# Kernel tuning notes

Hardware: AMD Instinct MI355X
Metric: run time of the kernel (lower is better)

The kernel has to match this reference:

```python
import jax, jax.numpy as jnp
import numpy as np

HEAD_NUM = 16


def setup_inputs() -> dict:
    key = jax.random.key(0)
    k1, k2, k3, k4 = jax.random.split(key, 4)
    B, S, E = 8, 1024, 1024
    inputs = jax.random.normal(k1, (B, S, E), dtype=jnp.float32)
    W_Query = jax.random.normal(k2, (E, E), dtype=jnp.float32) * 0.05
    W_Key = jax.random.normal(k3, (E, E), dtype=jnp.float32) * 0.05
    W_Value = jax.random.normal(k4, (E, E), dtype=jnp.float32) * 0.05
    return {"inputs": inputs, "W_Query": W_Query, "W_Key": W_Key, "W_Value": W_Value}


def reference(inputs, W_Query, W_Key, W_Value):
    B, S, E = inputs.shape
    H = HEAD_NUM
    D = E // H
    # QKV projections: [B,S,E] @ [E,E] -> [B,S,E]
    q = jnp.einsum('bse,ef->bsf', inputs, W_Query).reshape(B, S, H, D)
    k = jnp.einsum('bse,ef->bsf', inputs, W_Key).reshape(B, S, H, D)
    v = jnp.einsum('bse,ef->bsf', inputs, W_Value).reshape(B, S, H, D)
    # NOTE: original has NO 1/sqrt(D) scaling.
    scores = jnp.einsum('bihd,bjhd->bhij', q, k)  # [B,H,S,S]
    att = jax.nn.softmax(scores, axis=-1)
    out = jnp.einsum('bhij,bjhd->bihd', att, v).reshape(B, S, E)
    return jax.nn.relu(out)
```

## Files before the change

### kernel.cpp

```cpp
#include <hip/hip_runtime.h>
#include <cstdint>
#include <cstddef>

#define B_ 8
#define S_ 1024
#define E_ 1024
#define H_ 16
#define D_ 64
#define M_ (B_*S_)

typedef _Float16 f16;
typedef __attribute__((ext_vector_type(8))) _Float16 f16x8;
typedef __attribute__((ext_vector_type(4))) _Float16 f16x4;
typedef __attribute__((ext_vector_type(4))) float  f32x4;
typedef __attribute__((ext_vector_type(16))) float f32x16;
typedef __attribute__((ext_vector_type(4))) int    int4v;
typedef __attribute__((ext_vector_type(2))) int    int2v;

__device__ __forceinline__ f32x4 mfma16(f16x8 a, f16x8 b, f32x4 c) {
  return __builtin_amdgcn_mfma_f32_16x16x32_f16(a, b, c, 0, 0, 0);
}
__device__ __forceinline__ f32x16 mfma32(f16x8 a, f16x8 b, f32x16 c) {
  return __builtin_amdgcn_mfma_f32_32x32x16_f16(a, b, c, 0, 0, 0);
}
__device__ __forceinline__ void gll16(const f16* g, f16* l) {
  __builtin_amdgcn_global_load_lds(
      (const __attribute__((address_space(1))) void*)g,
      (__attribute__((address_space(3))) void*)l, 16, 0, 0);
}
__device__ __forceinline__ int pkrtz(float lo, float hi) {
  return __builtin_bit_cast(int, __builtin_amdgcn_cvt_pkrtz(lo, hi));
}

__global__ __launch_bounds__(256) void presplit_kernel(
    const float* __restrict__ X, f16* __restrict__ Xf) {
  size_t i = ((size_t)blockIdx.x * 256 + threadIdx.x) * 8;
  f32x4 v0 = *(const f32x4*)&X[i];
  f32x4 v1 = *(const f32x4*)&X[i + 4];
  f16x8 hv;
#pragma unroll
  for (int j = 0; j < 4; ++j) {
    hv[j] = (f16)v0[j];
    hv[j + 4] = (f16)v1[j];
  }
  *(f16x8*)&Xf[i] = hv;
}

__global__ __launch_bounds__(512) void wt_conv3_kernel(
    const float* __restrict__ Wq, const float* __restrict__ Wk,
    const float* __restrict__ Wv, f16* __restrict__ oq, f16* __restrict__ ok,
    f16* __restrict__ ov) {
  const float* W = blockIdx.z == 0 ? Wq : (blockIdx.z == 1 ? Wk : Wv);
  f16* o = blockIdx.z == 0 ? oq : (blockIdx.z == 1 ? ok : ov);
  const float scl = blockIdx.z == 0 ? 1.4426950408889634f : 1.0f;
  __shared__ float t[64][65];
  const int f0 = blockIdx.x * 64, e0 = blockIdx.y * 64;
  const int tx = threadIdx.x, ty = threadIdx.y;
#pragma unroll
  for (int j = 0; j < 8; ++j)
    t[ty + 8 * j][tx] = W[(size_t)(e0 + ty + 8 * j) * E_ + f0 + tx];
  __syncthreads();
#pragma unroll
  for (int j = 0; j < 8; ++j)
    o[(size_t)(f0 + ty + 8 * j) * E_ + e0 + tx] =
        (f16)(t[tx][ty + 8 * j] * scl);
}

__global__ __launch_bounds__(256) void gemm_qkv_kernel(
    const f16* __restrict__ Xf,
    const f16* __restrict__ Wq, const f16* __restrict__ Wk,
    const f16* __restrict__ Wv,
    f16* __restrict__ Qf, f16* __restrict__ Kf, f16* __restrict__ Vt) {
  __shared__ f16 sA[128][64], sB[128][64];
  const int bid = blockIdx.x;
  const int xcd = bid & 7, idx = bid >> 3;
  const int mb = xcd * 8 + idx / 24;
  const int nb = idx % 24;
  const int z = nb >> 3;
  const int n0 = (nb & 7) * 128, m0 = mb * 128;
  const f16* __restrict__ Bt = z == 0 ? Wq : (z == 1 ? Wk : Wv);
  const int tid = threadIdx.x;
  const int lane = tid & 63, w = tid >> 6;
  const int wm = (w >> 1) * 64, wn = (w & 1) * 64;
  const int fr = lane & 15, fg = lane >> 4;
  f32x4 acc[4][4] = {};
  for (int k0 = 0; k0 < E_; k0 += 64) {
#pragma unroll
    for (int i = 0; i < 4; ++i) {
      int ci = tid + i * 256;
      int r = ci >> 3, cl = ci & 7;
      int cs = (cl ^ (r & 7)) * 8;
      gll16(Xf + (size_t)(m0 + r) * E_ + k0 + cs, &sA[0][0] + ci * 8);
      gll16(Bt + (size_t)(n0 + r) * E_ + k0 + cs, &sB[0][0] + ci * 8);
    }
    __syncthreads();
#pragma unroll
    for (int kh2 = 0; kh2 < 2; ++kh2) {
      f16x8 ah[4];
#pragma unroll
      for (int mi = 0; mi < 4; ++mi) {
        int rA = wm + mi * 16 + fr;
        ah[mi] = *(const f16x8*)&sA[rA][(((kh2 * 4 + fg) ^ (rA & 7))) * 8];
      }
#pragma unroll
      for (int ni = 0; ni < 4; ++ni) {
        int rB = wn + ni * 16 + fr;
        f16x8 bh = *(const f16x8*)&sB[rB][(((kh2 * 4 + fg) ^ (rB & 7))) * 8];
#pragma unroll
        for (int mi = 0; mi < 4; ++mi)
          acc[mi][ni] = mfma16(ah[mi], bh, acc[mi][ni]);
      }
    }
    __syncthreads();
  }
  if (z < 2) {
    f16* Of = z == 0 ? Qf : Kf;
#pragma unroll
    for (int mi = 0; mi < 4; ++mi)
#pragma unroll
      for (int ni = 0; ni < 4; ++ni)
#pragma unroll
        for (int r = 0; r < 4; ++r) {
          int row = m0 + wm + mi * 16 + (lane >> 4) * 4 + r;
          int col = n0 + wn + ni * 16 + fr;
          int bb = row >> 10, s = row & 1023;
          int hd = col >> 6, d = col & 63;
          Of[((size_t)(bb * H_ + hd) * S_ + s) * D_ + d] = (f16)acc[mi][ni][r];
        }
  } else {
#pragma unroll
    for (int mi = 0; mi < 4; ++mi)
#pragma unroll
      for (int ni = 0; ni < 4; ++ni) {
        int row = m0 + wm + mi * 16 + (lane >> 4) * 4;
        int col = n0 + wn + ni * 16 + fr;
        int bb = row >> 10, s = row & 1023;
        int hd = col >> 6, d = col & 63;
        f16x4 p;
#pragma unroll
        for (int r = 0; r < 4; ++r) p[r] = (f16)acc[mi][ni][r];
        *(f16x4*)&Vt[((size_t)(bb * H_ + hd) * D_ + d) * S_ + s] = p;
      }
  }
}

__global__ __launch_bounds__(256, 4) void attn_kernel(
    const f16* __restrict__ Qf, const f16* __restrict__ Kf,
    const f16* __restrict__ Vt, float* __restrict__ out) {
  __shared__ f16 sK[2][64][64], sV[2][64][64];
  const int bid = blockIdx.x;
  const int bh = (bid & 7) * 16 + (bid >> 6);
  const int qb = (bid >> 3) & 7;
  const int hd = bh & 15, bb = bh >> 4;
  const int tid = threadIdx.x;
  const int lane = tid & 63, w = tid >> 6;
  const int cq = lane & 31, h = lane >> 5;
  const int rsw = cq & 7;
  const size_t base = (size_t)bh * (S_ * D_);
  const f16* Qf_p = Qf + base;
  const f16* Kf_p = Kf + base;
  const f16* Vt_p = Vt + base;
  const int q0 = qb * 128 + w * 32;

  f16x8 qh_[4];
#pragma unroll
  for (int ks = 0; ks < 4; ++ks)
    qh_[ks] = *(const f16x8*)&Qf_p[(size_t)(q0 + cq) * D_ + ks * 16 + 8 * h];

  f16x8 ones;
#pragma unroll
  for (int j = 0; j < 8; ++j) ones[j] = (f16)1.0f;

  float m_run;
  f32x16 O[2] = {}, Ol = {};
  f16x8 pf[4];

#define STAGE(buf, kb)                                                        \
  {                                                                           \
    _Pragma("unroll")                                                         \
    for (int half = 0; half < 2; ++half) {                                    \
      int ci = tid + half * 256;                                              \
      int row = ci >> 3, cl = ci & 7;                                         \
      int cs = cl ^ (row & 7);                                                \
      gll16(Kf_p + (size_t)((kb) + row) * D_ + cs * 8, &sK[buf][0][0] + ci * 8); \
      gll16(Vt_p + (size_t)row * S_ + (kb) + cs * 8, &sV[buf][0][0] + ci * 8);   \
    }                                                                         \
  }

#define QKT(scv, bufi)                                                        \
  {                                                                           \
    _Pragma("unroll")                                                         \
    for (int f = 0; f < 2; ++f) {                                             \
      _Pragma("unroll")                                                       \
      for (int ks = 0; ks < 4; ++ks) {                                        \
        int cc = ((2 * ks + h) ^ rsw) * 8;                                    \
        f16x8 kv = *(const f16x8*)&sK[bufi][f * 32 + cq][cc];                 \
        scv[f] = mfma32(kv, qh_[ks], scv[f]);                                 \
      }                                                                       \
    }                                                                         \
  }

#define MAXTREE(pm, scv)                                                      \
  {                                                                           \
    float t4[4];                                                              \
    _Pragma("unroll")                                                         \
    for (int i = 0; i < 4; ++i) {                                             \
      float a = fmaxf(fmaxf(scv[0][i], scv[0][i + 4]),                        \
                      fmaxf(scv[0][i + 8], scv[0][i + 12]));                  \
      float b = fmaxf(fmaxf(scv[1][i], scv[1][i + 4]),                        \
                      fmaxf(scv[1][i + 8], scv[1][i + 12]));                  \
      t4[i] = fmaxf(a, b);                                                    \
    }                                                                         \
    pm = fmaxf(fmaxf(t4[0], t4[1]), fmaxf(t4[2], t4[3]));                     \
    pm = fmaxf(pm, __shfl_xor(pm, 32));                                       \
  }

#define PFBUILD(scv)                                                          \
  {                                                                           \
    _Pragma("unroll")                                                         \
    for (int f = 0; f < 2; ++f) {                                             \
      _Pragma("unroll")                                                       \
      for (int ksl = 0; ksl < 2; ++ksl) {                                     \
        int b0 = 8 * ksl;                                                     \
        int a1 = pkrtz(scv[f][b0 + 0], scv[f][b0 + 1]);                       \
        int b1 = pkrtz(scv[f][b0 + 4], scv[f][b0 + 5]);                       \
        int2v r1 = __builtin_amdgcn_permlane32_swap(a1, b1, false, false);    \
        int a2 = pkrtz(scv[f][b0 + 2], scv[f][b0 + 3]);                       \
        int b2 = pkrtz(scv[f][b0 + 6], scv[f][b0 + 7]);                       \
        int2v r2 = __builtin_amdgcn_permlane32_swap(a2, b2, false, false);    \
        int4v wd;                                                             \
        wd[0] = r1[0]; wd[1] = r2[0]; wd[2] = r1[1]; wd[3] = r2[1];           \
        pf[2 * f + ksl] = __builtin_bit_cast(f16x8, wd);                      \
      }                                                                       \
    }                                                                         \
  }

#define PVT(bufi)                                                             \
  {                                                                           \
    _Pragma("unroll")                                                         \
    for (int ks = 0; ks < 4; ++ks) {                                          \
      int cc = ((2 * ks + h) ^ rsw) * 8;                                      \
      _Pragma("unroll")                                                       \
      for (int df = 0; df < 2; ++df) {                                        \
        f16x8 vf = *(const f16x8*)&sV[bufi][df * 32 + cq][cc];                \
        O[df] = mfma32(vf, pf[ks], O[df]);                                    \
      }                                                                       \
      Ol = mfma32(ones, pf[ks], Ol);                                          \
    }                                                                         \
  }

  STAGE(0, 0);
  asm volatile("s_waitcnt vmcnt(0)" ::: "memory");
  __builtin_amdgcn_sched_barrier(0);
  __builtin_amdgcn_s_barrier();
  STAGE(1, 64);
  {
    f32x16 sc[2] = {};
    __builtin_amdgcn_s_setprio(1);
    QKT(sc, 0);
    __builtin_amdgcn_s_setprio(0);
    float pm;
    MAXTREE(pm, sc);
    m_run = pm;
#pragma unroll
    for (int f = 0; f < 2; ++f)
#pragma unroll
      for (int r = 0; r < 16; ++r)
        sc[f][r] = __builtin_amdgcn_exp2f(sc[f][r] - pm);
    PFBUILD(sc);
    __builtin_amdgcn_s_setprio(1);
    PVT(0);
    __builtin_amdgcn_s_setprio(0);
  }
  asm volatile("s_waitcnt vmcnt(0)" ::: "memory");
  __builtin_amdgcn_sched_barrier(0);
  __builtin_amdgcn_s_barrier();

  for (int t = 1; t < 16; ++t) {
    const int cur = t & 1;
    if (t < 15) STAGE(cur ^ 1, (t + 1) * 64);

    f32x16 sc[2];
#pragma unroll
    for (int f = 0; f < 2; ++f)
#pragma unroll
      for (int r = 0; r < 16; ++r) sc[f][r] = -m_run;
    __builtin_amdgcn_s_setprio(1);
    QKT(sc, cur);
    __builtin_amdgcn_s_setprio(0);

#pragma unroll
    for (int f = 0; f < 2; ++f)
#pragma unroll
      for (int r = 0; r < 16; ++r)
        sc[f][r] = __builtin_amdgcn_exp2f(sc[f][r]);

    float pm;
    MAXTREE(pm, sc);
    if (__any(pm > 2048.f)) {
      float pmx = fmaxf(pm, 1.0f);
      float scl = 1.0f / pmx;
      m_run += __builtin_amdgcn_logf(pmx);
#pragma unroll
      for (int f = 0; f < 2; ++f)
#pragma unroll
        for (int r = 0; r < 16; ++r) sc[f][r] *= scl;
#pragma unroll
      for (int df = 0; df < 2; ++df)
#pragma unroll
        for (int i = 0; i < 16; ++i) O[df][i] *= scl;
#pragma unroll
      for (int i = 0; i < 16; ++i) Ol[i] *= scl;
    }

    PFBUILD(sc);
    __builtin_amdgcn_s_setprio(1);
    PVT(cur);
    __builtin_amdgcn_s_setprio(0);

    asm volatile("s_waitcnt vmcnt(0)" ::: "memory");
    __builtin_amdgcn_sched_barrier(0);
    __builtin_amdgcn_s_barrier();
  }

  float inv = 1.0f / Ol[0];
  int s = q0 + cq;
  float* orow = out + ((size_t)bb * S_ + s) * E_ + hd * 64;
#pragma unroll
  for (int df = 0; df < 2; ++df)
#pragma unroll
    for (int g = 0; g < 4; ++g) {
      f32x4 vv;
#pragma unroll
      for (int j = 0; j < 4; ++j)
        vv[j] = fmaxf(O[df][4 * g + j] * inv, 0.f);
      *(f32x4*)&orow[df * 32 + 8 * g + 4 * h] = vv;
    }
}

extern "C" void kernel_launch(void* const* d_in, const int* in_sizes, int n_in,
                              void* d_out, int out_size, void* d_ws, size_t ws_size,
                              hipStream_t stream) {
  const float* X  = (const float*)d_in[0];
  const float* Wq = (const float*)d_in[1];
  const float* Wk = (const float*)d_in[2];
  const float* Wv = (const float*)d_in[3];
  float* out = (float*)d_out;
  char* ws = (char*)d_ws;

  const size_t WSZ = (size_t)E_ * E_ * sizeof(f16);
  const size_t QSZ = (size_t)M_ * E_ * sizeof(f16);
  f16* Wqf = (f16*)(ws);
  f16* Wkf = (f16*)(ws + WSZ);
  f16* Wvf = (f16*)(ws + 2 * WSZ);
  char* p = ws + 3 * WSZ;
  f16* Xf = (f16*)(p);
  f16* Qf = (f16*)(p + QSZ);
  f16* Kf = (f16*)(p + 2 * QSZ);
  f16* Vt = (f16*)(p + 3 * QSZ);

  presplit_kernel<<<4096, 256, 0, stream>>>(X, Xf);
  wt_conv3_kernel<<<dim3(16, 16, 3), dim3(64, 8), 0, stream>>>(
      Wq, Wk, Wv, Wqf, Wkf, Wvf);

  gemm_qkv_kernel<<<1536, 256, 0, stream>>>(
      Xf, Wqf, Wkf, Wvf, Qf, Kf, Vt);

  attn_kernel<<<1024, 256, 0, stream>>>(Qf, Kf, Vt, out);
}
```

Measured before the change: 132.7 us.

## Merge prep kernels into one launch and compute softmax row sum with VALU

The X fp16 conversion and the weight transpose/convert kernels are combined into a single launch, with block ranges dispatching to each job, removing one kernel launch and its tail. In attention, the softmax denominator was previously computed by an extra MFMA against a ones vector each tile. It is now a VALU row-sum of the fp32 probabilities plus a cross-half shuffle. This frees matrix-core work but adds VALU adds, and the sum is now taken over fp32 values rather than the fp16-rounded values used in P·V.

```diff
diff --git a/kernel.cpp b/kernel.cpp
--- a/kernel.cpp
+++ b/kernel.cpp
@@ -32,38 +32,44 @@
   return __builtin_bit_cast(int, __builtin_amdgcn_cvt_pkrtz(lo, hi));
 }
 
-__global__ __launch_bounds__(256) void presplit_kernel(
-    const float* __restrict__ X, f16* __restrict__ Xf) {
-  size_t i = ((size_t)blockIdx.x * 256 + threadIdx.x) * 8;
-  f32x4 v0 = *(const f32x4*)&X[i];
-  f32x4 v1 = *(const f32x4*)&X[i + 4];
-  f16x8 hv;
-#pragma unroll
-  for (int j = 0; j < 4; ++j) {
-    hv[j] = (f16)v0[j];
-    hv[j + 4] = (f16)v1[j];
-  }
-  *(f16x8*)&Xf[i] = hv;
-}
-
-__global__ __launch_bounds__(512) void wt_conv3_kernel(
-    const float* __restrict__ Wq, const float* __restrict__ Wk,
-    const float* __restrict__ Wv, f16* __restrict__ oq, f16* __restrict__ ok,
+__global__ __launch_bounds__(256) void prep_kernel(
+    const float* __restrict__ X, const float* __restrict__ Wq,
+    const float* __restrict__ Wk, const float* __restrict__ Wv,
+    f16* __restrict__ Xf, f16* __restrict__ oq, f16* __restrict__ ok,
     f16* __restrict__ ov) {
-  const float* W = blockIdx.z == 0 ? Wq : (blockIdx.z == 1 ? Wk : Wv);
-  f16* o = blockIdx.z == 0 ? oq : (blockIdx.z == 1 ? ok : ov);
-  const float scl = blockIdx.z == 0 ? 1.4426950408889634f : 1.0f;
   __shared__ float t[64][65];
-  const int f0 = blockIdx.x * 64, e0 = blockIdx.y * 64;
-  const int tx = threadIdx.x, ty = threadIdx.y;
-#pragma unroll
-  for (int j = 0; j < 8; ++j)
-    t[ty + 8 * j][tx] = W[(size_t)(e0 + ty + 8 * j) * E_ + f0 + tx];
+  const int bid = blockIdx.x;
+  if (bid < 4096) {
+    size_t i = ((size_t)bid * 256 + threadIdx.x) * 8;
+    f32x4 v0 = *(const f32x4*)&X[i];
+    f32x4 v1 = *(const f32x4*)&X[i + 4];
+    f16x8 hv;
+#pragma unroll
+    for (int j = 0; j < 4; ++j) {
+      hv[j] = (f16)v0[j];
+      hv[j + 4] = (f16)v1[j];
+    }
+    *(f16x8*)&Xf[i] = hv;
+    return;
+  }
+  const int wid = bid - 4096;
+  const int which = wid >> 8, tile = wid & 255;
+  const float* W = which == 0 ? Wq : (which == 1 ? Wk : Wv);
+  f16* o = which == 0 ? oq : (which == 1 ? ok : ov);
+  const float scl = which == 0 ? 1.4426950408889634f : 1.0f;
+  const int f0 = (tile & 15) * 64, e0 = (tile >> 4) * 64;
+  const int tx = threadIdx.x & 63, tyy = threadIdx.x >> 6;
+#pragma unroll
+  for (int j = 0; j < 16; ++j) {
+    int row = 4 * j + tyy;
+    t[row][tx] = W[(size_t)(e0 + row) * E_ + f0 + tx];
+  }
   __syncthreads();
 #pragma unroll
-  for (int j = 0; j < 8; ++j)
-    o[(size_t)(f0 + ty + 8 * j) * E_ + e0 + tx] =
-        (f16)(t[tx][ty + 8 * j] * scl);
+  for (int j = 0; j < 16; ++j) {
+    int row = 4 * j + tyy;
+    o[(size_t)(f0 + row) * E_ + e0 + tx] = (f16)(t[tx][row] * scl);
+  }
 }
 
 __global__ __launch_bounds__(256) void gemm_qkv_kernel(
@@ -167,12 +173,8 @@
   for (int ks = 0; ks < 4; ++ks)
     qh_[ks] = *(const f16x8*)&Qf_p[(size_t)(q0 + cq) * D_ + ks * 16 + 8 * h];
 
-  f16x8 ones;
-#pragma unroll
-  for (int j = 0; j < 8; ++j) ones[j] = (f16)1.0f;
-
-  float m_run;
-  f32x16 O[2] = {}, Ol = {};
+  float m_run, l_run;
+  f32x16 O[2] = {};
   f16x8 pf[4];
 
 #define STAGE(buf, kb)                                                        \
@@ -213,6 +215,23 @@
     }                                                                         \
     pm = fmaxf(fmaxf(t4[0], t4[1]), fmaxf(t4[2], t4[3]));                     \
     pm = fmaxf(pm, __shfl_xor(pm, 32));                                       \
+  }
+
+#define ROWSUM(rs, scv)                                                       \
+  {                                                                           \
+    float rs0 = 0.f, rs1 = 0.f, rs2 = 0.f, rs3 = 0.f;                         \
+    _Pragma("unroll")                                                         \
+    for (int f = 0; f < 2; ++f) {                                             \
+      _Pragma("unroll")                                                       \
+      for (int r4 = 0; r4 < 4; ++r4) {                                        \
+        rs0 += scv[f][4 * r4 + 0];                                            \
+        rs1 += scv[f][4 * r4 + 1];                                            \
+        rs2 += scv[f][4 * r4 + 2];                                            \
+        rs3 += scv[f][4 * r4 + 3];                                            \
+      }                                                                       \
+    }                                                                         \
+    rs = (rs0 + rs1) + (rs2 + rs3);                                           \
+    rs += __shfl_xor(rs, 32);                                                 \
   }
 
 #define PFBUILD(scv)                                                          \
@@ -245,7 +264,6 @@
         f16x8 vf = *(const f16x8*)&sV[bufi][df * 32 + cq][cc];                \
         O[df] = mfma32(vf, pf[ks], O[df]);                                    \
       }                                                                       \
-      Ol = mfma32(ones, pf[ks], Ol);                                          \
     }                                                                         \
   }
 
@@ -267,6 +285,9 @@
 #pragma unroll
       for (int r = 0; r < 16; ++r)
         sc[f][r] = __builtin_amdgcn_exp2f(sc[f][r] - pm);
+    float rs;
+    ROWSUM(rs, sc);
+    l_run = rs;
     PFBUILD(sc);
     __builtin_amdgcn_s_setprio(1);
     PVT(0);
@@ -301,6 +322,7 @@
       float pmx = fmaxf(pm, 1.0f);
       float scl = 1.0f / pmx;
       m_run += __builtin_amdgcn_logf(pmx);
+      l_run *= scl;
 #pragma unroll
       for (int f = 0; f < 2; ++f)
 #pragma unroll
@@ -309,10 +331,11 @@
       for (int df = 0; df < 2; ++df)
 #pragma unroll
         for (int i = 0; i < 16; ++i) O[df][i] *= scl;
-#pragma unroll
-      for (int i = 0; i < 16; ++i) Ol[i] *= scl;
-    }
-
+    }
+
+    float rs;
+    ROWSUM(rs, sc);
+    l_run += rs;
     PFBUILD(sc);
     __builtin_amdgcn_s_setprio(1);
     PVT(cur);
@@ -323,7 +346,7 @@
     __builtin_amdgcn_s_barrier();
   }
 
-  float inv = 1.0f / Ol[0];
+  float inv = 1.0f / l_run;
   int s = q0 + cq;
   float* orow = out + ((size_t)bb * S_ + s) * E_ + hd * 64;
 #pragma unroll
@@ -359,9 +382,7 @@
   f16* Kf = (f16*)(p + 2 * QSZ);
   f16* Vt = (f16*)(p + 3 * QSZ);
 
-  presplit_kernel<<<4096, 256, 0, stream>>>(X, Xf);
-  wt_conv3_kernel<<<dim3(16, 16, 3), dim3(64, 8), 0, stream>>>(
-      Wq, Wk, Wv, Wqf, Wkf, Wvf);
+  prep_kernel<<<4864, 256, 0, stream>>>(X, Wq, Wk, Wv, Xf, Wqf, Wkf, Wvf);
 
   gemm_qkv_kernel<<<1536, 256, 0, stream>>>(
       Xf, Wqf, Wkf, Wvf, Qf, Kf, Vt);
```

Result: no change. 133.5 us (+0.6%).
